# Kernel optimization log

Measured on AMD Instinct MI355X. Metric: run time of the kernel, lower is better.

The kernel has to match this reference:

```python
import jax, jax.numpy as jnp
import numpy as np

D_MODEL, N_HEADS, D_HEAD = 768, 12, 64
BATCH, SEQ = 4, 2048
INIT_STD = 0.02


def setup_inputs() -> dict:
    key = jax.random.key(0)
    ks = jax.random.split(key, 5)
    x = jax.random.normal(ks[0], (BATCH, SEQ, D_MODEL), dtype=jnp.float32)
    W_Q = INIT_STD * jax.random.normal(ks[1], (N_HEADS, D_MODEL, D_HEAD), dtype=jnp.float32)
    W_K = INIT_STD * jax.random.normal(ks[2], (N_HEADS, D_MODEL, D_HEAD), dtype=jnp.float32)
    W_V = INIT_STD * jax.random.normal(ks[3], (N_HEADS, D_MODEL, D_HEAD), dtype=jnp.float32)
    W_O = INIT_STD * jax.random.normal(ks[4], (N_HEADS, D_HEAD, D_MODEL), dtype=jnp.float32)
    b_Q = jnp.zeros((N_HEADS, D_HEAD), dtype=jnp.float32)
    b_K = jnp.zeros((N_HEADS, D_HEAD), dtype=jnp.float32)
    b_V = jnp.zeros((N_HEADS, D_HEAD), dtype=jnp.float32)
    b_O = jnp.zeros((D_MODEL,), dtype=jnp.float32)
    return {"x": x, "W_Q": W_Q, "W_K": W_K, "W_V": W_V, "W_O": W_O,
            "b_Q": b_Q, "b_K": b_K, "b_V": b_V, "b_O": b_O}


def reference(x, W_Q, W_K, W_V, W_O, b_Q, b_K, b_V, b_O):
    # projections: [b,s,e] x [n,e,h] -> [b,s,n,h]
    q = jnp.einsum('bse,neh->bsnh', x, W_Q) + b_Q
    k = jnp.einsum('bse,neh->bsnh', x, W_K) + b_K
    v = jnp.einsum('bse,neh->bsnh', x, W_V) + b_V
    scores = jnp.einsum('bqnh,bknh->bnqk', q, k) / np.float32(np.sqrt(D_HEAD))
    S = x.shape[1]
    causal = jnp.tril(jnp.ones((S, S), dtype=bool))  # True where allowed
    scores = jnp.where(causal, scores, -jnp.inf)
    pattern = jax.nn.softmax(scores, axis=-1)
    z = jnp.einsum('bnqk,bknh->bqnh', pattern, v)
    # combine heads: sum over n of z @ W_O
    attn_out = jnp.einsum('bqnh,nhe->bqe', z, W_O) + b_O
    return attn_out
```

## Files before the change

kernel.cpp:

```cpp
#include <hip/hip_runtime.h>
#include <hip/hip_bf16.h>

typedef short s16x8 __attribute__((ext_vector_type(8)));
typedef short s16x4 __attribute__((ext_vector_type(4)));
typedef float f32x4 __attribute__((ext_vector_type(4)));
typedef __hip_bfloat16 bf16;

#define MFMA16(a, b, c) __builtin_amdgcn_mfma_f32_16x16x32_bf16((a), (b), (c), 0, 0, 0)

#define BATCH 4
#define SEQ 2048
#define NH 12
#define DH 64
#define DM 768
#define ROWS (BATCH * SEQ)
#define QKVC (3 * DM)
#define LOG2E 1.4426950408889634f

static __device__ inline float fast_exp2(float x) {
  float r;
  asm("v_exp_f32 %0, %1" : "=v"(r) : "v"(x));
  return r;
}
static __device__ inline unsigned pkbf16(float a, float b) {
  bf16 ha = __float2bfloat16(a), hb = __float2bfloat16(b);
  unsigned short ua, ub;
  __builtin_memcpy(&ua, &ha, 2);
  __builtin_memcpy(&ub, &hb, 2);
  return (unsigned)ua | ((unsigned)ub << 16);
}

typedef __attribute__((address_space(3))) unsigned int lds_u32;
typedef __attribute__((address_space(1))) const unsigned int glb_u32;
static __device__ inline void gl2lds16(const void* g, void* l) {
  __builtin_amdgcn_global_load_lds((glb_u32*)g, (lds_u32*)l, 16, 0, 0);
}

#define NWC (QKVC * DM)
#define NWO (DM * DM)
#define NXC (ROWS * DM / 8)
__global__ __launch_bounds__(256) void prep_all(
    const float* __restrict__ wq, const float* __restrict__ wk,
    const float* __restrict__ wv, const float* __restrict__ wo,
    const float* __restrict__ x, bf16* __restrict__ WcT,
    bf16* __restrict__ WoT, bf16* __restrict__ xb) {
  int i = blockIdx.x * 256 + threadIdx.x;
  if (i < NWC) {
    int c = i / DM, e = i % DM;
    int mat = c / DM;
    int r = c % DM;
    int n = r >> 6, h = r & 63;
    const float* W = (mat == 0) ? wq : ((mat == 1) ? wk : wv);
    WcT[i] = __float2bfloat16(W[n * (DM * DH) + e * DH + h]);
  } else if (i < NWC + NWO) {
    int j = i - NWC;
    int e = j / DM, r = j % DM;
    WoT[j] = __float2bfloat16(wo[r * DM + e]);
  } else {
    int j = i - NWC - NWO;
    const float* src = x + (size_t)j * 8;
    float4 f0 = *(const float4*)src;
    float4 f1 = *(const float4*)(src + 4);
    bf16 tmp[8];
    tmp[0] = __float2bfloat16(f0.x); tmp[1] = __float2bfloat16(f0.y);
    tmp[2] = __float2bfloat16(f0.z); tmp[3] = __float2bfloat16(f0.w);
    tmp[4] = __float2bfloat16(f1.x); tmp[5] = __float2bfloat16(f1.y);
    tmp[6] = __float2bfloat16(f1.z); tmp[7] = __float2bfloat16(f1.w);
    *(s16x8*)(xb + (size_t)j * 8) = *(const s16x8*)tmp;
  }
}

__global__ __launch_bounds__(256) void qkv_gemm(
    const bf16* __restrict__ xb, const bf16* __restrict__ WcT,
    const float* __restrict__ bQ, const float* __restrict__ bK,
    const float* __restrict__ bV, bf16* __restrict__ Qb,
    bf16* __restrict__ Kb, bf16* __restrict__ Vt) {
  __shared__ bf16 As[128 * 32];
  __shared__ bf16 Bs[128 * 32];
  const int m0 = blockIdx.x * 128;
  const int n0 = blockIdx.y * 128;
  const int tid = threadIdx.x;
  const int wave = tid >> 6, lane = tid & 63;
  const int quad = lane >> 4, l15 = lane & 15;
  const int wm = (wave & 1) * 64, wn = (wave >> 1) * 64;

  f32x4 acc[4][4] = {};

  for (int k0 = 0; k0 < DM; k0 += 32) {
    {
      int c = tid, row = c >> 2, sg = (c & 3) << 3;
      gl2lds16(xb + (size_t)(m0 + row) * DM + k0 + sg, &As[c * 8]);
      gl2lds16(WcT + (size_t)(n0 + row) * DM + k0 + sg, &Bs[c * 8]);
      c = tid + 256; row = c >> 2; sg = (c & 3) << 3;
      gl2lds16(xb + (size_t)(m0 + row) * DM + k0 + sg, &As[c * 8]);
      gl2lds16(WcT + (size_t)(n0 + row) * DM + k0 + sg, &Bs[c * 8]);
    }
    __syncthreads();
    s16x8 af[4], bfr[4];
    for (int i = 0; i < 4; i++)
      af[i] = *(const s16x8*)&As[(wm + i * 16 + l15) * 32 + quad * 8];
    for (int j = 0; j < 4; j++)
      bfr[j] = *(const s16x8*)&Bs[(wn + j * 16 + l15) * 32 + quad * 8];
    for (int i = 0; i < 4; i++)
      for (int j = 0; j < 4; j++)
        acc[i][j] = MFMA16(af[i], bfr[j], acc[i][j]);
    __syncthreads();
  }

  const int mat = n0 / DM;
  for (int j = 0; j < 4; j++) {
    int col = n0 + wn + j * 16 + l15;
    int cc = col - mat * DM;
    int head = cc >> 6, h = cc & 63;
    float bsv = ((mat == 0) ? bQ : (mat == 1) ? bK : bV)[cc];
    for (int i = 0; i < 4; i++) {
      int row0 = m0 + wm + i * 16 + quad * 4;
      int b = row0 >> 11;
      int s = row0 & 2047;
      int bh = b * NH + head;
      if (mat == 2) {
        s16x4 pv;
        for (int r = 0; r < 4; r++) {
          bf16 hv = __float2bfloat16(acc[i][j][r] + bsv);
          short sv; __builtin_memcpy(&sv, &hv, 2);
          pv[r] = sv;
        }
        *(s16x4*)(Vt + ((size_t)bh * DH + h) * SEQ + s) = pv;
      } else {
        const float scale = (mat == 0) ? (0.125f * LOG2E) : 1.0f;
        bf16* dst = ((mat == 0) ? Qb : Kb) + ((size_t)bh * SEQ + s) * DH + h;
        for (int r = 0; r < 4; r++)
          dst[(size_t)r * DH] = __float2bfloat16((acc[i][j][r] + bsv) * scale);
      }
    }
  }
}

__global__ __launch_bounds__(256) void flash_kernel(
    const bf16* __restrict__ Qb, const bf16* __restrict__ Kb,
    const bf16* __restrict__ Vt, bf16* __restrict__ Z) {
  __shared__ bf16 Ks[64 * 72];
  __shared__ bf16 VsT[64 * 72];
  __shared__ bf16 Ps[4][16 * 72];

  const int bh = blockIdx.x >> 4;
  const int p = blockIdx.x & 15;
  const int qtA = 31 - p, qtB = p;
  const int b = bh / NH, head = bh % NH;
  const int tid = threadIdx.x;
  const int wave = tid >> 6, lane = tid & 63;
  const int quad = lane >> 4, l15 = lane & 15;
  const int qwA = qtA * 64 + wave * 16;
  const int qwB = qtB * 64 + wave * 16;

  const bf16* Kbase = Kb + (size_t)bh * SEQ * DH;
  const bf16* Vbase = Vt + (size_t)bh * DH * SEQ;

  s16x8 bqA[2], bqB[2];
  for (int ks = 0; ks < 2; ks++) {
    bqA[ks] = *(const s16x8*)(Qb +
        ((size_t)bh * SEQ + qwA + l15) * DH + ks * 32 + quad * 8);
    bqB[ks] = *(const s16x8*)(Qb +
        ((size_t)bh * SEQ + qwB + l15) * DH + ks * 32 + quad * 8);
  }

  f32x4 oA[4] = {}, oB[4] = {};
  float lA = 0.f, lB = 0.f;

  s16x8 kr[2], vr[2];
  auto load_tile = [&](int kt) {
    const int kbase = kt * 64;
    for (int u = 0; u < 2; u++) {
      int c = tid + u * 256;
      int row = c >> 3, seg = (c & 7) << 3;
      kr[u] = *(const s16x8*)(Kbase + (size_t)(kbase + row) * DH + seg);
      vr[u] = *(const s16x8*)(Vbase + (size_t)row * SEQ + kbase + seg);
    }
  };
  auto store_tile = [&]() {
    for (int u = 0; u < 2; u++) {
      int c = tid + u * 256;
      int row = c >> 3, seg = (c & 7) << 3;
      *(s16x8*)&Ks[row * 72 + seg] = kr[u];
      *(s16x8*)&VsT[row * 72 + seg] = vr[u];
    }
  };

  auto compute = [&](int kt, const s16x8 bq[2], f32x4 o[4], float& l_i,
                     int qw, bool diag) {
    const int kbase = kt * 64;
    f32x4 s[4] = {};
    for (int ks = 0; ks < 2; ks++) {
      s16x8 ak[4];
      for (int ktf = 0; ktf < 4; ktf++)
        ak[ktf] = *(const s16x8*)&Ks[(ktf * 16 + l15) * 72 + ks * 32 + quad * 8];
      for (int ktf = 0; ktf < 4; ktf++)
        s[ktf] = MFMA16(ak[ktf], bq[ks], s[ktf]);
    }

    if (diag) {
      int qg = qw + l15;
      for (int ktf = 0; ktf < 4; ktf++)
        for (int r = 0; r < 4; r++) {
          int kg = kbase + ktf * 16 + quad * 4 + r;
          if (kg > qg) s[ktf][r] = -1e30f;
        }
    }

    float rs = 0.f;
    for (int ktf = 0; ktf < 4; ktf++)
      for (int r = 0; r < 4; r++) {
        float pv = fast_exp2(s[ktf][r]);
        s[ktf][r] = pv;
        rs += pv;
      }
    l_i += rs;

    bf16* Pw = Ps[wave];
    for (int ktf = 0; ktf < 4; ktf++) {
      uint2 w;
      w.x = pkbf16(s[ktf][0], s[ktf][1]);
      w.y = pkbf16(s[ktf][2], s[ktf][3]);
      *(uint2*)&Pw[l15 * 72 + ktf * 16 + quad * 4] = w;
    }
    asm volatile("s_waitcnt lgkmcnt(0)" ::: "memory");

    for (int ks2 = 0; ks2 < 2; ks2++) {
      s16x8 ap = *(const s16x8*)&Pw[l15 * 72 + ks2 * 32 + quad * 8];
      for (int hf = 0; hf < 4; hf++) {
        s16x8 bv =
            *(const s16x8*)&VsT[(hf * 16 + l15) * 72 + ks2 * 32 + quad * 8];
        o[hf] = MFMA16(ap, bv, o[hf]);
      }
    }
  };

  load_tile(0);
  for (int kt = 0; kt <= qtA; kt++) {
    __syncthreads();
    store_tile();
    __syncthreads();
    if (kt < qtA) load_tile(kt + 1);
    compute(kt, bqA, oA, lA, qwA, kt == qtA);
    if (kt <= qtB) compute(kt, bqB, oB, lB, qwB, kt == qtB);
  }

  auto epilogue = [&](f32x4 o[4], float l_i, int qw) {
    float lv = l_i;
    lv += __shfl_xor(lv, 16, 64);
    lv += __shfl_xor(lv, 32, 64);
    float linv = 1.f / lv;
    for (int r = 0; r < 4; r++) {
      float li = __shfl(linv, (lane & 48) | (quad * 4 + r), 64);
      int q = qw + quad * 4 + r;
      for (int hf = 0; hf < 4; hf++) {
        Z[((size_t)b * SEQ + q) * DM + head * DH + hf * 16 + l15] =
            __float2bfloat16(o[hf][r] * li);
      }
    }
  };
  epilogue(oA, lA, qwA);
  epilogue(oB, lB, qwB);
}

__global__ __launch_bounds__(256) void out_gemm(
    const bf16* __restrict__ Z, const bf16* __restrict__ WoT,
    const float* __restrict__ bO, float* __restrict__ out) {
  __shared__ bf16 As[128 * 32];
  __shared__ bf16 Bs[128 * 32];
  const int m0 = blockIdx.x * 128;
  const int n0 = blockIdx.y * 128;
  const int tid = threadIdx.x;
  const int wave = tid >> 6, lane = tid & 63;
  const int quad = lane >> 4, l15 = lane & 15;
  const int wm = (wave & 1) * 64, wn = (wave >> 1) * 64;

  f32x4 acc[4][4] = {};

  for (int k0 = 0; k0 < DM; k0 += 32) {
    {
      int c = tid, row = c >> 2, sg = (c & 3) << 3;
      gl2lds16(Z + (size_t)(m0 + row) * DM + k0 + sg, &As[c * 8]);
      gl2lds16(WoT + (size_t)(n0 + row) * DM + k0 + sg, &Bs[c * 8]);
      c = tid + 256; row = c >> 2; sg = (c & 3) << 3;
      gl2lds16(Z + (size_t)(m0 + row) * DM + k0 + sg, &As[c * 8]);
      gl2lds16(WoT + (size_t)(n0 + row) * DM + k0 + sg, &Bs[c * 8]);
    }
    __syncthreads();
    s16x8 af[4], bfr[4];
    for (int i = 0; i < 4; i++)
      af[i] = *(const s16x8*)&As[(wm + i * 16 + l15) * 32 + quad * 8];
    for (int j = 0; j < 4; j++)
      bfr[j] = *(const s16x8*)&Bs[(wn + j * 16 + l15) * 32 + quad * 8];
    for (int i = 0; i < 4; i++)
      for (int j = 0; j < 4; j++)
        acc[i][j] = MFMA16(af[i], bfr[j], acc[i][j]);
    __syncthreads();
  }

  for (int j = 0; j < 4; j++) {
    int col = n0 + wn + j * 16 + l15;
    float bv = bO[col];
    for (int i = 0; i < 4; i++)
      for (int r = 0; r < 4; r++) {
        int row = m0 + wm + i * 16 + quad * 4 + r;
        out[(size_t)row * DM + col] = acc[i][j][r] + bv;
      }
  }
}

extern "C" void kernel_launch(void* const* d_in, const int* in_sizes, int n_in,
                              void* d_out, int out_size, void* d_ws,
                              size_t ws_size, hipStream_t stream) {
  const float* x  = (const float*)d_in[0];
  const float* wq = (const float*)d_in[1];
  const float* wk = (const float*)d_in[2];
  const float* wv = (const float*)d_in[3];
  const float* wo = (const float*)d_in[4];
  const float* bq = (const float*)d_in[5];
  const float* bk = (const float*)d_in[6];
  const float* bv = (const float*)d_in[7];
  const float* bo = (const float*)d_in[8];
  float* out = (float*)d_out;

  bf16* WcT = (bf16*)d_ws;
  bf16* WoT = WcT + (size_t)QKVC * DM;
  bf16* Qb  = WoT + (size_t)DM * DM;
  bf16* Kb  = Qb + (size_t)ROWS * DM;
  bf16* Vt  = Kb + (size_t)ROWS * DM;
  bf16* xbZ = Vt + (size_t)ROWS * DM;

  prep_all<<<(NWC + NWO + NXC) / 256, 256, 0, stream>>>(
      wq, wk, wv, wo, x, WcT, WoT, xbZ);
  qkv_gemm<<<dim3(ROWS / 128, QKVC / 128), 256, 0, stream>>>(
      xbZ, WcT, bq, bk, bv, Qb, Kb, Vt);
  flash_kernel<<<48 * 16, 256, 0, stream>>>(Qb, Kb, Vt, xbZ);
  out_gemm<<<dim3(ROWS / 128, DM / 128), 256, 0, stream>>>(xbZ, WoT, bo, out);
}
```

Measured before the change: 219.3 us.

## Double-buffer flash K/V via direct LDS loads and widen GEMM K-tiles

The flash kernel now double-buffers the K and V tiles in LDS, filling them with direct global-to-LDS loads instead of staging through registers. This removes one barrier per iteration and lets the next tile's load overlap with compute. Both GEMMs now step K by 64 rather than 32, halving the number of barriers. The output GEMM also uses 64-row M tiles so more blocks launch. In exchange, LDS rows lose their 72-element padding, which may cause bank conflicts on the fragment reads.

```diff
diff --git a/kernel.cpp b/kernel.cpp
--- a/kernel.cpp
+++ b/kernel.cpp
@@ -75,8 +75,8 @@
     const float* __restrict__ bQ, const float* __restrict__ bK,
     const float* __restrict__ bV, bf16* __restrict__ Qb,
     bf16* __restrict__ Kb, bf16* __restrict__ Vt) {
-  __shared__ bf16 As[128 * 32];
-  __shared__ bf16 Bs[128 * 32];
+  __shared__ bf16 As[128 * 64];
+  __shared__ bf16 Bs[128 * 64];
   const int m0 = blockIdx.x * 128;
   const int n0 = blockIdx.y * 128;
   const int tid = threadIdx.x;
@@ -86,24 +86,24 @@
 
   f32x4 acc[4][4] = {};
 
-  for (int k0 = 0; k0 < DM; k0 += 32) {
-    {
-      int c = tid, row = c >> 2, sg = (c & 3) << 3;
+  for (int k0 = 0; k0 < DM; k0 += 64) {
+    for (int u = 0; u < 4; u++) {
+      int c = tid + u * 256;
+      int row = c >> 3, sg = (c & 7) << 3;
       gl2lds16(xb + (size_t)(m0 + row) * DM + k0 + sg, &As[c * 8]);
       gl2lds16(WcT + (size_t)(n0 + row) * DM + k0 + sg, &Bs[c * 8]);
-      c = tid + 256; row = c >> 2; sg = (c & 3) << 3;
-      gl2lds16(xb + (size_t)(m0 + row) * DM + k0 + sg, &As[c * 8]);
-      gl2lds16(WcT + (size_t)(n0 + row) * DM + k0 + sg, &Bs[c * 8]);
-    }
-    __syncthreads();
-    s16x8 af[4], bfr[4];
-    for (int i = 0; i < 4; i++)
-      af[i] = *(const s16x8*)&As[(wm + i * 16 + l15) * 32 + quad * 8];
-    for (int j = 0; j < 4; j++)
-      bfr[j] = *(const s16x8*)&Bs[(wn + j * 16 + l15) * 32 + quad * 8];
-    for (int i = 0; i < 4; i++)
+    }
+    __syncthreads();
+    for (int ks = 0; ks < 2; ks++) {
+      s16x8 af[4], bfr[4];
+      for (int i = 0; i < 4; i++)
+        af[i] = *(const s16x8*)&As[(wm + i * 16 + l15) * 64 + ks * 32 + quad * 8];
       for (int j = 0; j < 4; j++)
-        acc[i][j] = MFMA16(af[i], bfr[j], acc[i][j]);
+        bfr[j] = *(const s16x8*)&Bs[(wn + j * 16 + l15) * 64 + ks * 32 + quad * 8];
+      for (int i = 0; i < 4; i++)
+        for (int j = 0; j < 4; j++)
+          acc[i][j] = MFMA16(af[i], bfr[j], acc[i][j]);
+    }
     __syncthreads();
   }
 
@@ -139,8 +139,8 @@
 __global__ __launch_bounds__(256) void flash_kernel(
     const bf16* __restrict__ Qb, const bf16* __restrict__ Kb,
     const bf16* __restrict__ Vt, bf16* __restrict__ Z) {
-  __shared__ bf16 Ks[64 * 72];
-  __shared__ bf16 VsT[64 * 72];
+  __shared__ bf16 Ks[2][64 * 64];
+  __shared__ bf16 VsT[2][64 * 64];
   __shared__ bf16 Ps[4][16 * 72];
 
   const int bh = blockIdx.x >> 4;
@@ -167,33 +167,25 @@
   f32x4 oA[4] = {}, oB[4] = {};
   float lA = 0.f, lB = 0.f;
 
-  s16x8 kr[2], vr[2];
-  auto load_tile = [&](int kt) {
+  auto stage_tile = [&](int kt, int buf) {
     const int kbase = kt * 64;
     for (int u = 0; u < 2; u++) {
       int c = tid + u * 256;
       int row = c >> 3, seg = (c & 7) << 3;
-      kr[u] = *(const s16x8*)(Kbase + (size_t)(kbase + row) * DH + seg);
-      vr[u] = *(const s16x8*)(Vbase + (size_t)row * SEQ + kbase + seg);
+      gl2lds16(Kbase + (size_t)(kbase + row) * DH + seg, &Ks[buf][c * 8]);
+      gl2lds16(Vbase + (size_t)row * SEQ + kbase + seg, &VsT[buf][c * 8]);
     }
   };
-  auto store_tile = [&]() {
-    for (int u = 0; u < 2; u++) {
-      int c = tid + u * 256;
-      int row = c >> 3, seg = (c & 7) << 3;
-      *(s16x8*)&Ks[row * 72 + seg] = kr[u];
-      *(s16x8*)&VsT[row * 72 + seg] = vr[u];
-    }
-  };
-
-  auto compute = [&](int kt, const s16x8 bq[2], f32x4 o[4], float& l_i,
-                     int qw, bool diag) {
+
+  auto compute = [&](int kt, int buf, const s16x8 bq[2], f32x4 o[4],
+                     float& l_i, int qw, bool diag) {
     const int kbase = kt * 64;
     f32x4 s[4] = {};
     for (int ks = 0; ks < 2; ks++) {
       s16x8 ak[4];
       for (int ktf = 0; ktf < 4; ktf++)
-        ak[ktf] = *(const s16x8*)&Ks[(ktf * 16 + l15) * 72 + ks * 32 + quad * 8];
+        ak[ktf] =
+            *(const s16x8*)&Ks[buf][(ktf * 16 + l15) * 64 + ks * 32 + quad * 8];
       for (int ktf = 0; ktf < 4; ktf++)
         s[ktf] = MFMA16(ak[ktf], bq[ks], s[ktf]);
     }
@@ -229,20 +221,19 @@
       s16x8 ap = *(const s16x8*)&Pw[l15 * 72 + ks2 * 32 + quad * 8];
       for (int hf = 0; hf < 4; hf++) {
         s16x8 bv =
-            *(const s16x8*)&VsT[(hf * 16 + l15) * 72 + ks2 * 32 + quad * 8];
+            *(const s16x8*)&VsT[buf][(hf * 16 + l15) * 64 + ks2 * 32 + quad * 8];
         o[hf] = MFMA16(ap, bv, o[hf]);
       }
     }
   };
 
-  load_tile(0);
+  stage_tile(0, 0);
   for (int kt = 0; kt <= qtA; kt++) {
-    __syncthreads();
-    store_tile();
-    __syncthreads();
-    if (kt < qtA) load_tile(kt + 1);
-    compute(kt, bqA, oA, lA, qwA, kt == qtA);
-    if (kt <= qtB) compute(kt, bqB, oB, lB, qwB, kt == qtB);
+    const int cur = kt & 1;
+    __syncthreads();
+    if (kt < qtA) stage_tile(kt + 1, cur ^ 1);
+    compute(kt, cur, bqA, oA, lA, qwA, kt == qtA);
+    if (kt <= qtB) compute(kt, cur, bqB, oB, lB, qwB, kt == qtB);
   }
 
   auto epilogue = [&](f32x4 o[4], float l_i, int qw) {
@@ -266,42 +257,46 @@
 __global__ __launch_bounds__(256) void out_gemm(
     const bf16* __restrict__ Z, const bf16* __restrict__ WoT,
     const float* __restrict__ bO, float* __restrict__ out) {
-  __shared__ bf16 As[128 * 32];
-  __shared__ bf16 Bs[128 * 32];
-  const int m0 = blockIdx.x * 128;
+  __shared__ bf16 As[64 * 64];
+  __shared__ bf16 Bs[128 * 64];
+  const int m0 = blockIdx.x * 64;
   const int n0 = blockIdx.y * 128;
   const int tid = threadIdx.x;
   const int wave = tid >> 6, lane = tid & 63;
   const int quad = lane >> 4, l15 = lane & 15;
-  const int wm = (wave & 1) * 64, wn = (wave >> 1) * 64;
-
-  f32x4 acc[4][4] = {};
-
-  for (int k0 = 0; k0 < DM; k0 += 32) {
-    {
-      int c = tid, row = c >> 2, sg = (c & 3) << 3;
+  const int wm = (wave & 1) * 32, wn = (wave >> 1) * 64;
+
+  f32x4 acc[2][4] = {};
+
+  for (int k0 = 0; k0 < DM; k0 += 64) {
+    for (int u = 0; u < 2; u++) {
+      int c = tid + u * 256;
+      int row = c >> 3, sg = (c & 7) << 3;
       gl2lds16(Z + (size_t)(m0 + row) * DM + k0 + sg, &As[c * 8]);
+    }
+    for (int u = 0; u < 4; u++) {
+      int c = tid + u * 256;
+      int row = c >> 3, sg = (c & 7) << 3;
       gl2lds16(WoT + (size_t)(n0 + row) * DM + k0 + sg, &Bs[c * 8]);
-      c = tid + 256; row = c >> 2; sg = (c & 3) << 3;
-      gl2lds16(Z + (size_t)(m0 + row) * DM + k0 + sg, &As[c * 8]);
-      gl2lds16(WoT + (size_t)(n0 + row) * DM + k0 + sg, &Bs[c * 8]);
-    }
-    __syncthreads();
-    s16x8 af[4], bfr[4];
-    for (int i = 0; i < 4; i++)
-      af[i] = *(const s16x8*)&As[(wm + i * 16 + l15) * 32 + quad * 8];
-    for (int j = 0; j < 4; j++)
-      bfr[j] = *(const s16x8*)&Bs[(wn + j * 16 + l15) * 32 + quad * 8];
-    for (int i = 0; i < 4; i++)
+    }
+    __syncthreads();
+    for (int ks = 0; ks < 2; ks++) {
+      s16x8 af[2], bfr[4];
+      for (int i = 0; i < 2; i++)
+        af[i] = *(const s16x8*)&As[(wm + i * 16 + l15) * 64 + ks * 32 + quad * 8];
       for (int j = 0; j < 4; j++)
-        acc[i][j] = MFMA16(af[i], bfr[j], acc[i][j]);
+        bfr[j] = *(const s16x8*)&Bs[(wn + j * 16 + l15) * 64 + ks * 32 + quad * 8];
+      for (int i = 0; i < 2; i++)
+        for (int j = 0; j < 4; j++)
+          acc[i][j] = MFMA16(af[i], bfr[j], acc[i][j]);
+    }
     __syncthreads();
   }
 
   for (int j = 0; j < 4; j++) {
     int col = n0 + wn + j * 16 + l15;
     float bv = bO[col];
-    for (int i = 0; i < 4; i++)
+    for (int i = 0; i < 2; i++)
       for (int r = 0; r < 4; r++) {
         int row = m0 + wm + i * 16 + quad * 4 + r;
         out[(size_t)row * DM + col] = acc[i][j][r] + bv;
@@ -335,5 +330,5 @@
   qkv_gemm<<<dim3(ROWS / 128, QKVC / 128), 256, 0, stream>>>(
       xbZ, WcT, bq, bk, bv, Qb, Kb, Vt);
   flash_kernel<<<48 * 16, 256, 0, stream>>>(Qb, Kb, Vt, xbZ);
-  out_gemm<<<dim3(ROWS / 128, DM / 128), 256, 0, stream>>>(xbZ, WoT, bo, out);
-}
+  out_gemm<<<dim3(ROWS / 64, DM / 128), 256, 0, stream>>>(xbZ, WoT, bo, out);
+}
```

Result: slower. 253.1 us (+15.4%).

## Double-buffer K/V tiles with direct global-to-LDS loads in flash kernel

Applied to the files above, without the earlier changes.

Replaces the register-staged K/V tile loads with direct global-to-LDS transfers (gl2lds16) into two alternating shared-memory buffers. The next tile is fetched while the current one is computed, so each iteration needs one barrier instead of two. This doubles K/V LDS use and relies on the barrier also waiting for the outstanding async loads. The copy loop now moves 9 segments per padded row, the ninth filling padding with duplicate data, which adds a little extra traffic.

```diff
diff --git a/kernel.cpp b/kernel.cpp
--- a/kernel.cpp
+++ b/kernel.cpp
@@ -139,8 +139,8 @@
 __global__ __launch_bounds__(256) void flash_kernel(
     const bf16* __restrict__ Qb, const bf16* __restrict__ Kb,
     const bf16* __restrict__ Vt, bf16* __restrict__ Z) {
-  __shared__ bf16 Ks[64 * 72];
-  __shared__ bf16 VsT[64 * 72];
+  __shared__ bf16 Ks[2][64 * 72];
+  __shared__ bf16 VsT[2][64 * 72];
   __shared__ bf16 Ps[4][16 * 72];
 
   const int bh = blockIdx.x >> 4;
@@ -167,33 +167,30 @@
   f32x4 oA[4] = {}, oB[4] = {};
   float lA = 0.f, lB = 0.f;
 
-  s16x8 kr[2], vr[2];
-  auto load_tile = [&](int kt) {
+  auto stage_tile = [&](int kt, int buf) {
     const int kbase = kt * 64;
-    for (int u = 0; u < 2; u++) {
+    for (int u = 0; u < 3; u++) {
       int c = tid + u * 256;
-      int row = c >> 3, seg = (c & 7) << 3;
-      kr[u] = *(const s16x8*)(Kbase + (size_t)(kbase + row) * DH + seg);
-      vr[u] = *(const s16x8*)(Vbase + (size_t)row * SEQ + kbase + seg);
+      if (c < 576) {
+        int row = (c * 57345) >> 19;
+        row = c / 9;
+        int i = c - row * 9;
+        int off = (i & 7) << 3;
+        gl2lds16(Kbase + (size_t)(kbase + row) * DH + off, &Ks[buf][c * 8]);
+        gl2lds16(Vbase + (size_t)row * SEQ + kbase + off, &VsT[buf][c * 8]);
+      }
     }
   };
-  auto store_tile = [&]() {
-    for (int u = 0; u < 2; u++) {
-      int c = tid + u * 256;
-      int row = c >> 3, seg = (c & 7) << 3;
-      *(s16x8*)&Ks[row * 72 + seg] = kr[u];
-      *(s16x8*)&VsT[row * 72 + seg] = vr[u];
-    }
-  };
-
-  auto compute = [&](int kt, const s16x8 bq[2], f32x4 o[4], float& l_i,
-                     int qw, bool diag) {
+
+  auto compute = [&](int kt, int buf, const s16x8 bq[2], f32x4 o[4],
+                     float& l_i, int qw, bool diag) {
     const int kbase = kt * 64;
     f32x4 s[4] = {};
     for (int ks = 0; ks < 2; ks++) {
       s16x8 ak[4];
       for (int ktf = 0; ktf < 4; ktf++)
-        ak[ktf] = *(const s16x8*)&Ks[(ktf * 16 + l15) * 72 + ks * 32 + quad * 8];
+        ak[ktf] =
+            *(const s16x8*)&Ks[buf][(ktf * 16 + l15) * 72 + ks * 32 + quad * 8];
       for (int ktf = 0; ktf < 4; ktf++)
         s[ktf] = MFMA16(ak[ktf], bq[ks], s[ktf]);
     }
@@ -229,20 +226,19 @@
       s16x8 ap = *(const s16x8*)&Pw[l15 * 72 + ks2 * 32 + quad * 8];
       for (int hf = 0; hf < 4; hf++) {
         s16x8 bv =
-            *(const s16x8*)&VsT[(hf * 16 + l15) * 72 + ks2 * 32 + quad * 8];
+            *(const s16x8*)&VsT[buf][(hf * 16 + l15) * 72 + ks2 * 32 + quad * 8];
         o[hf] = MFMA16(ap, bv, o[hf]);
       }
     }
   };
 
-  load_tile(0);
+  stage_tile(0, 0);
   for (int kt = 0; kt <= qtA; kt++) {
-    __syncthreads();
-    store_tile();
-    __syncthreads();
-    if (kt < qtA) load_tile(kt + 1);
-    compute(kt, bqA, oA, lA, qwA, kt == qtA);
-    if (kt <= qtB) compute(kt, bqB, oB, lB, qwB, kt == qtB);
+    const int cur = kt & 1;
+    __syncthreads();
+    if (kt < qtA) stage_tile(kt + 1, cur ^ 1);
+    compute(kt, cur, bqA, oA, lA, qwA, kt == qtA);
+    if (kt <= qtB) compute(kt, cur, bqB, oB, lB, qwB, kt == qtB);
   }
 
   auto epilogue = [&](f32x4 o[4], float l_i, int qw) {
```

Result: slower. 226.0 us (+3.0%).
